# Kernel optimization log

Hardware: AMD Instinct MI355X
Metric: run time of the kernel (lower is better)

The kernel has to match this reference:

```python
import jax, jax.numpy as jnp
import numpy as np

S, G, N, E = 4, 3, 20000, 320000   # seq_len, num_graphs, nodes, edges
DIN = HID = OUT = 64


def setup_inputs() -> dict:
    key = jax.random.key(0)
    ks = jax.random.split(key, 12)
    s = 0.1  # weight scale ~ Glorot-ish for d=64
    return {
        "x": jax.random.normal(ks[0], (S, G, N, DIN), jnp.float32),
        "edge_index": jax.random.randint(ks[1], (S, G, 2, E), 0, N, dtype=jnp.int32),
        "W1l": jax.random.normal(ks[2], (G, DIN, HID), jnp.float32) * s,
        "W1r": jax.random.normal(ks[3], (G, DIN, HID), jnp.float32) * s,
        "b1": jnp.zeros((G, HID), jnp.float32),
        "W2l": jax.random.normal(ks[4], (G, HID, OUT), jnp.float32) * s,
        "W2r": jax.random.normal(ks[5], (G, HID, OUT), jnp.float32) * s,
        "b2": jnp.zeros((G, OUT), jnp.float32),
        "Wih": jax.random.normal(ks[6], (4 * OUT, OUT), jnp.float32) * s,
        "Whh": jax.random.normal(ks[7], (4 * OUT, OUT), jnp.float32) * s,
        "bih": jnp.zeros((4 * OUT,), jnp.float32),
        "bhh": jnp.zeros((4 * OUT,), jnp.float32),
    }


def _sage(x, ei, Wl, Wr, b):
    # PyG SAGEConv(aggr='mean'): out = mean_{j->i}(x_j) @ Wl + x_i @ Wr + b
    src, dst = ei[0], ei[1]
    n = x.shape[0]
    msg = jax.ops.segment_sum(x[src], dst, num_segments=n)          # [N, d]
    cnt = jax.ops.segment_sum(jnp.ones((ei.shape[1], 1), x.dtype), dst, num_segments=n)
    mean = jnp.where(cnt > 0, msg / jnp.maximum(cnt, 1.0), 0.0)
    return mean @ Wl + x @ Wr + b


def _gnn(x, ei, Wl1, Wr1, bb1, Wl2, Wr2, bb2):
    h = jnp.tanh(_sage(x, ei, Wl1, Wr1, bb1))
    return jnp.tanh(_sage(h, ei, Wl2, Wr2, bb2))


def reference(x, edge_index, W1l, W1r, b1, W2l, W2r, b2, Wih, Whh, bih, bhh):
    # vmap over graphs (each graph has its own conv weights), then over timesteps
    per_graph = jax.vmap(_gnn, in_axes=(0, 0, 0, 0, 0, 0, 0, 0))
    per_seq = jax.vmap(per_graph, in_axes=(0, 0, None, None, None, None, None, None))
    h = per_seq(x, edge_index, W1l, W1r, b1, W2l, W2r, b2)          # [S, G, N, OUT]
    # torch: per timestep stack graphs [G,N,O] -> transpose -> [N,G,O]; cat over seq on dim0
    lstm_in = jnp.transpose(h, (0, 2, 1, 3)).reshape(S * N, G, OUT)  # [B, T=G, OUT]
    B = lstm_in.shape[0]

    def step(carry, xt):
        hp, cp = carry
        gates = xt @ Wih.T + hp @ Whh.T + bih + bhh                 # [B, 4*OUT]
        i, f, g, o = jnp.split(gates, 4, axis=-1)                   # torch gate order i,f,g,o
        c = jax.nn.sigmoid(f) * cp + jax.nn.sigmoid(i) * jnp.tanh(g)
        hn = jax.nn.sigmoid(o) * jnp.tanh(c)
        return (hn, c), None

    init = (jnp.zeros((B, OUT), x.dtype), jnp.zeros((B, OUT), x.dtype))
    (h_last, _), _ = jax.lax.scan(step, init, jnp.transpose(lstm_in, (1, 0, 2)))
    return h_last  # [S*N, OUT] == lstm_out[:, -1, :].squeeze()
```

## Files before the change

### kernel.cpp

```cpp
#include <hip/hip_runtime.h>
#include <math.h>

#define S 4
#define G 3
#define NN 20000
#define EE 320000
#define D 64
#define SG (S*G)

#define RGS 32
#define RNODES2 625
#define BCAP 14336
#define CHUNKA 100

#define LTILES 313
#define LTASKS (12*LTILES)
#define LQ (LTASKS/8)
#define LR (LTASKS%8)
#define NGRP   (NN/16)

static __device__ __forceinline__ float rcpf(float x){ return __builtin_amdgcn_rcpf(x); }
static __device__ __forceinline__ float sigmf(float x){ return rcpf(1.0f + __expf(-x)); }
static __device__ __forceinline__ float tanhf_fast(float x){
    float t = __expf(2.0f*x);
    return 1.0f - 2.0f*rcpf(t + 1.0f);
}

static __device__ __forceinline__ unsigned short f2bf(float f){
    union { float f; unsigned u; } v; v.f = f;
    unsigned r = v.u + 0x7FFF + ((v.u >> 16) & 1);
    return (unsigned short)(r >> 16);
}

typedef short bf16x8 __attribute__((ext_vector_type(8)));
typedef float f32x4  __attribute__((ext_vector_type(4)));


__global__ __launch_bounds__(256) void binA_kernel(const int* __restrict__ ei,
                                                   int* __restrict__ bcur,
                                                   int* __restrict__ bkt){
    __shared__ int wcnt[4*RGS];
    __shared__ int wb[4*RGS];
    int chunk = blockIdx.x, sg = blockIdx.y;
    int tid = threadIdx.x, w = tid >> 6;
    const int* srcp = ei + (size_t)(sg*2 + 0)*EE;
    const int* dstp = ei + (size_t)(sg*2 + 1)*EE;
    const int EPC = EE/CHUNKA;
    int start = chunk*EPC, end = start + EPC;

    for (int it = 0; it < (EPC + 1023)/1024; ++it){
        if (tid < 4*RGS) wcnt[tid] = 0;
        __syncthreads();
        int e = start + it*1024 + tid*4;
        bool valid = e < end;
        int d_[4], s_[4], r_[4], dl_[4], rk_[4];
        if (valid){
            int4 d4 = *(const int4*)&dstp[e];
            int4 s4 = *(const int4*)&srcp[e];
            d_[0]=d4.x; d_[1]=d4.y; d_[2]=d4.z; d_[3]=d4.w;
            s_[0]=s4.x; s_[1]=s4.y; s_[2]=s4.z; s_[3]=s4.w;
            #pragma unroll
            for (int j = 0; j < 4; ++j){
                int r = d_[j] / RNODES2;
                r_[j]  = r;
                dl_[j] = d_[j] - r*RNODES2;
                rk_[j] = atomicAdd(&wcnt[w*RGS + r], 1);
            }
        }
        __syncthreads();
        if (tid < RGS){
            int c0 = wcnt[0*RGS+tid], c1 = wcnt[1*RGS+tid];
            int c2 = wcnt[2*RGS+tid], c3 = wcnt[3*RGS+tid];
            int tot = c0+c1+c2+c3;
            int gb = 0;
            if (tot > 0) gb = atomicAdd(&bcur[sg*RGS + tid], tot);
            wb[0*RGS+tid] = gb;
            wb[1*RGS+tid] = gb + c0;
            wb[2*RGS+tid] = gb + c0 + c1;
            wb[3*RGS+tid] = gb + c0 + c1 + c2;
        }
        __syncthreads();
        if (valid){
            #pragma unroll
            for (int j = 0; j < 4; ++j){
                int pos = wb[w*RGS + r_[j]] + rk_[j];
                if (pos < BCAP)
                    bkt[(size_t)(sg*RGS + r_[j])*BCAP + pos] = (dl_[j] << 15) | s_[j];
            }
        }
    }
}


__global__ __launch_bounds__(256) void buildB_kernel(int* __restrict__ bkt,
                                                     const int* __restrict__ bcur,
                                                     int* __restrict__ off2,
                                                     int* __restrict__ deg2,
                                                     int* __restrict__ nid2,
                                                     int* __restrict__ offU){
    __shared__ int hist[RNODES2];
    __shared__ int pref[RNODES2];
    __shared__ int seg[BCAP];
    __shared__ int sums[256];
    __shared__ int dh[64];
    int sg = blockIdx.x / RGS, rg = blockIdx.x % RGS;
    int tid = threadIdx.x;
    int cnt = bcur[sg*RGS + rg];
    if (cnt > BCAP) cnt = BCAP;
    size_t base = (size_t)(sg*RGS + rg)*BCAP;
    int gnode = sg*NN + rg*RNODES2;

    for (int i = tid; i < RNODES2; i += 256) hist[i] = 0;
    if (tid < 64) dh[tid] = 0;
    __syncthreads();
    for (int j = tid; j < cnt; j += 256)
        atomicAdd(&hist[bkt[base + j] >> 15], 1);
    __syncthreads();

    int lo = tid*3, hi = min(lo+3, RNODES2);
    int s = 0;
    for (int i = lo; i < hi; ++i) s += (hist[i] + 3) & ~3;
    sums[tid] = s; __syncthreads();
    for (int ofs = 1; ofs < 256; ofs <<= 1){
        int v = (tid >= ofs) ? sums[tid-ofs] : 0;
        __syncthreads();
        sums[tid] += v;
        __syncthreads();
    }
    int run = sums[tid] - s;
    for (int i = lo; i < hi; ++i){
        pref[i] = run;
        offU[gnode + i] = (int)base + run;
        run += (hist[i] + 3) & ~3;
    }
    __syncthreads();

    for (int i = tid; i < RNODES2; i += 256)
        atomicAdd(&dh[min(hist[i], 63)], 1);
    __syncthreads();
    if (tid == 0){
        int r = 0;
        for (int k = 0; k < 64; ++k){ int c = dh[k]; dh[k] = r; r += c; }
    }
    __syncthreads();
    for (int i = tid; i < RNODES2; i += 256){
        int pos = atomicAdd(&dh[min(hist[i], 63)], 1);
        off2[gnode + pos] = offU[gnode + i];
        deg2[gnode + pos] = hist[i];
        nid2[gnode + pos] = rg*RNODES2 + i;
    }
    __syncthreads();

    for (int j = tid; j < cnt; j += 256){
        int p = bkt[base + j];
        int slot = atomicAdd(&pref[p >> 15], 1);
        if (slot < BCAP) seg[slot] = p & 0x7FFF;
    }
    __syncthreads();

    int padtot = min(sums[255], BCAP);
    for (int j = tid; j < padtot; j += 256) bkt[base + j] = seg[j];
}


__global__ __launch_bounds__(256) void convert_kernel(const float* __restrict__ x,
                                                      unsigned short* __restrict__ xb){
    int idx = blockIdx.x*256 + threadIdx.x;
    if (idx >= SG*NN*16) return;
    float4 v = ((const float4*)x)[idx];
    uint2 pk;
    pk.x = (unsigned)f2bf(v.x) | ((unsigned)f2bf(v.y) << 16);
    pk.y = (unsigned)f2bf(v.z) | ((unsigned)f2bf(v.w) << 16);
    ((uint2*)xb)[idx] = pk;
}


__global__ __launch_bounds__(256) void wprep2_kernel(const float* __restrict__ W1l,
                                                     const float* __restrict__ W1r,
                                                     const float* __restrict__ W2l,
                                                     const float* __restrict__ W2r,
                                                     const float* __restrict__ Wih,
                                                     const float* __restrict__ Whh,
                                                     const float* __restrict__ bih,
                                                     const float* __restrict__ bhh,
                                                     unsigned short* __restrict__ WL1,
                                                     unsigned short* __restrict__ WL2,
                                                     unsigned short* __restrict__ Wt,
                                                     float* __restrict__ bc){
    int idx = blockIdx.x*256 + threadIdx.x;
    if (idx < 24576){
        int g = idx >> 13, rem = idx & 8191, col = rem >> 7, k = rem & 127;
        float v = (k < 64) ? W1l[((size_t)g*64 + k)*64 + col]
                           : W1r[((size_t)g*64 + (k-64))*64 + col];
        WL1[idx] = f2bf(v);
    } else if (idx < 49152){
        int t = idx - 24576;
        int g = t >> 13, rem = t & 8191, col = rem >> 7, k = rem & 127;
        float v = (k < 64) ? W2l[((size_t)g*64 + k)*64 + col]
                           : W2r[((size_t)g*64 + (k-64))*64 + col];
        WL2[t] = f2bf(v);
    } else if (idx < 81920){
        int t = idx - 49152;
        int col = t >> 7, k = t & 127;
        float v = (k < 64) ? Wih[col*64 + k] : Whh[col*64 + (k - 64)];
        Wt[t] = f2bf(v);
    } else if (idx < 82176){
        int t = idx - 81920;
        bc[t] = bih[t] + bhh[t];
    }
}


#define WP 72

#define LOADCH(F, IX, JB) { \
    int ii0_ = (IX).x, ii1_ = (IX).y, ii2_ = (IX).z, ii3_ = (IX).w; \
    unsigned o0_ = (((unsigned)ii0_) << 7) + qb; if ((JB) + 0 >= dg) o0_ = zoff; \
    unsigned o1_ = (((unsigned)ii1_) << 7) + qb; if ((JB) + 1 >= dg) o1_ = zoff; \
    unsigned o2_ = (((unsigned)ii2_) << 7) + qb; if ((JB) + 2 >= dg) o2_ = zoff; \
    unsigned o3_ = (((unsigned)ii3_) << 7) + qb; if ((JB) + 3 >= dg) o3_ = zoff; \
    F[0] = *(const bf16x8*)(inbc + o0_); F[1] = *(const bf16x8*)(inbc + o0_ + 64); \
    F[2] = *(const bf16x8*)(inbc + o1_); F[3] = *(const bf16x8*)(inbc + o1_ + 64); \
    F[4] = *(const bf16x8*)(inbc + o2_); F[5] = *(const bf16x8*)(inbc + o2_ + 64); \
    F[6] = *(const bf16x8*)(inbc + o3_); F[7] = *(const bf16x8*)(inbc + o3_ + 64); \
}

#define MFMAS(F) { \
    __builtin_amdgcn_s_setprio(1); \
    _Pragma("unroll") \
    for (int j_ = 0; j_ < 4; ++j_){ \
        _Pragma("unroll") \
        for (int ct_ = 0; ct_ < 4; ++ct_) \
            acc[ct_] = __builtin_amdgcn_mfma_f32_16x16x32_bf16(F[2*j_],   B0[ct_], acc[ct_], 0, 0, 0); \
        _Pragma("unroll") \
        for (int ct_ = 0; ct_ < 4; ++ct_) \
            acc[ct_] = __builtin_amdgcn_mfma_f32_16x16x32_bf16(F[2*j_+1], B1[ct_], acc[ct_], 0, 0, 0); \
    } \
    __builtin_amdgcn_s_setprio(0); \
}

__global__ __launch_bounds__(256,3) void layer_kernel(const unsigned short* __restrict__ xb,
                                                    const int* __restrict__ off2,
                                                    const int* __restrict__ deg2,
                                                    const int* __restrict__ nid2,
                                                    const int* __restrict__ csr,
                                                    const unsigned short* __restrict__ WL,
                                                    const float* __restrict__ bias,
                                                    unsigned short* __restrict__ outb){
    __shared__ unsigned short sO[4][16*WP];
    int L = blockIdx.x;
    int xcd = L & 7;
    int task = ((xcd < LR) ? xcd*(LQ+1) : LR*(LQ+1) + (xcd-LR)*LQ) + (L >> 3);
    int sg = task / LTILES;
    int tsel = task - sg*LTILES;
    int tile = (LTILES-1) - tsel;
    int g = sg % G;
    int tid = threadIdx.x;
    int wave = tid >> 6, lane = tid & 63;
    int r = lane & 15, q = lane >> 4;
    unsigned qb = (unsigned)(q << 4);
    const char* inbc = (const char*)(xb + (size_t)sg*NN*D);

    int gid = tile*4 + wave;
    bool wv = (gid < NGRP);

    const unsigned short* WLg = WL + (size_t)g*64*128;
    bf16x8 B0[4], B1[4];
    #pragma unroll
    for (int ct = 0; ct < 4; ++ct){
        B0[ct] = *(const bf16x8*)&WLg[(ct*16 + r)*128 + 0*32 + q*8];
        B1[ct] = *(const bf16x8*)&WLg[(ct*16 + r)*128 + 1*32 + q*8];
    }
    asm volatile("" : "+v"(B0[0]), "+v"(B0[1]), "+v"(B0[2]), "+v"(B0[3]),
                      "+v"(B1[0]), "+v"(B1[1]), "+v"(B1[2]), "+v"(B1[3]));

    int idx = sg*NN + gid*16 + r;
    int node = 0, dg = 0, a = 0;
    if (wv){
        node = nid2[idx];
        a    = off2[idx];
        dg   = deg2[idx];
    }
    int mx = dg;
    mx = max(mx, __shfl_xor(mx, 1));
    mx = max(mx, __shfl_xor(mx, 2));
    mx = max(mx, __shfl_xor(mx, 4));
    mx = max(mx, __shfl_xor(mx, 8));

    bf16x8 S0 = *(const bf16x8*)(inbc + (((unsigned)node) << 7) + qb);
    bf16x8 S1 = *(const bf16x8*)(inbc + (((unsigned)node) << 7) + qb + 64);

    unsigned zoff = (((unsigned)((SG - sg)*NN)) << 7) + qb;

    f32x4 acc[4];
    #pragma unroll
    for (int ct = 0; ct < 4; ++ct) acc[ct] = (f32x4){0.f,0.f,0.f,0.f};

    if (mx > 0){
        int4 ix0 = *(const int4*)&csr[a];
        int4 ix1 = *(const int4*)&csr[a + 4];
        bf16x8 FA[8], FB[8];
        LOADCH(FA, ix0, 0);
        LOADCH(FB, ix1, 4);
        ix0 = *(const int4*)&csr[a + 8];
        ix1 = *(const int4*)&csr[a + 12];
        int nch = (mx + 3) >> 2;
        for (int c = 0; c < nch; c += 2){
            MFMAS(FA);
            LOADCH(FA, ix0, (c + 2)*4);
            ix0 = *(const int4*)&csr[a + (c + 4)*4];
            if (c + 1 < nch){
                MFMAS(FB);
                LOADCH(FB, ix1, (c + 3)*4);
                ix1 = *(const int4*)&csr[a + (c + 5)*4];
            }
        }
    }

    float inv[4];
    #pragma unroll
    for (int reg = 0; reg < 4; ++reg){
        int d = __shfl(dg, (q << 2) | reg, 16);
        inv[reg] = (d > 0) ? rcpf((float)d) : 0.0f;
    }
    #pragma unroll
    for (int ct = 0; ct < 4; ++ct)
        #pragma unroll
        for (int reg = 0; reg < 4; ++reg)
            acc[ct][reg] *= inv[reg];

    #pragma unroll
    for (int ct = 0; ct < 4; ++ct){
        bf16x8 b2 = *(const bf16x8*)&WLg[(ct*16 + r)*128 + 2*32 + q*8];
        acc[ct] = __builtin_amdgcn_mfma_f32_16x16x32_bf16(S0, b2, acc[ct], 0, 0, 0);
        bf16x8 b3 = *(const bf16x8*)&WLg[(ct*16 + r)*128 + 3*32 + q*8];
        acc[ct] = __builtin_amdgcn_mfma_f32_16x16x32_bf16(S1, b3, acc[ct], 0, 0, 0);
    }

    #pragma unroll
    for (int ct = 0; ct < 4; ++ct){
        float bv = bias[g*64 + ct*16 + r];
        #pragma unroll
        for (int reg = 0; reg < 4; ++reg)
            sO[wave][(q*4+reg)*WP + ct*16 + r] = f2bf(tanhf_fast(acc[ct][reg] + bv));
    }
    if (wv){
        #pragma unroll
        for (int pass = 0; pass < 2; ++pass){
            int rloc = pass*8 + (lane >> 3), chunk = lane & 7;
            int i2 = gid*16 + rloc;
            int nd = nid2[sg*NN + i2];
            uint4 v = *(const uint4*)&sO[wave][rloc*WP + chunk*8];
            *(uint4*)&outb[((size_t)sg*NN + nd)*D + chunk*8] = v;
        }
    }
}


__global__ __launch_bounds__(256) void lstm_kernel(const unsigned short* __restrict__ h2b,
                                                   const unsigned short* __restrict__ Wt,
                                                   const float* __restrict__ bc,
                                                   float* __restrict__ out){
    __shared__ unsigned short sH[64*WP];
    int tid = threadIdx.x;
    int b0 = blockIdx.x * 64;
    int wave = tid >> 6, lane = tid & 63;
    int n0 = lane & 15, q = lane >> 4;
    int jcol = wave*16 + n0;

    float bb[4];
    #pragma unroll
    for (int T = 0; T < 4; ++T) bb[T] = bc[T*64 + jcol];

    float c[4][4];
    #pragma unroll
    for (int rt = 0; rt < 4; ++rt)
        #pragma unroll
        for (int reg = 0; reg < 4; ++reg) c[rt][reg] = 0.0f;

    int s_[4], n_[4];
    #pragma unroll
    for (int rt = 0; rt < 4; ++rt){
        int b = b0 + rt*16 + n0;
        s_[rt] = b / NN; n_[rt] = b - s_[rt]*NN;
    }

    #pragma unroll
    for (int t = 0; t < G; ++t){
        f32x4 accv[4][4];
        #pragma unroll
        for (int rt = 0; rt < 4; ++rt)
            #pragma unroll
            for (int T = 0; T < 4; ++T) accv[rt][T] = (f32x4){0.f,0.f,0.f,0.f};

        int nkc = (t == 0) ? 2 : 4;
        #pragma unroll
        for (int kc = 0; kc < 4; ++kc){
            if (kc >= nkc) break;
            bf16x8 af[4];
            #pragma unroll
            for (int rt = 0; rt < 4; ++rt){
                if (kc < 2) af[rt] = *(const bf16x8*)&h2b[((size_t)(s_[rt]*G + t)*NN + n_[rt])*D + kc*32 + q*8];
                else        af[rt] = *(const bf16x8*)&sH[(rt*16 + n0)*WP + (kc-2)*32 + q*8];
            }
            #pragma unroll
            for (int T = 0; T < 4; ++T){
                int ct = T*4 + wave;
                bf16x8 bfr = *(const bf16x8*)&Wt[(ct*16 + n0)*128 + kc*32 + q*8];
                #pragma unroll
                for (int rt = 0; rt < 4; ++rt)
                    accv[rt][T] = __builtin_amdgcn_mfma_f32_16x16x32_bf16(af[rt], bfr, accv[rt][T], 0, 0, 0);
            }
        }
        if (t > 0) __syncthreads();

        #pragma unroll
        for (int rt = 0; rt < 4; ++rt){
            #pragma unroll
            for (int reg = 0; reg < 4; ++reg){
                float ig = sigmf(accv[rt][0][reg] + bb[0]);
                float fg = sigmf(accv[rt][1][reg] + bb[1]);
                float gg = tanhf_fast(accv[rt][2][reg] + bb[2]);
                float og = sigmf(accv[rt][3][reg] + bb[3]);
                float cn = fg*c[rt][reg] + ig*gg;
                c[rt][reg] = cn;
                float hv = og * tanhf_fast(cn);
                int row = rt*16 + q*4 + reg;
                if (t < G-1) sH[row*WP + jcol] = f2bf(hv);
                else         out[(size_t)(b0 + row)*D + jcol] = hv;
            }
        }
        if (t < G-1) __syncthreads();
    }
}


extern "C" void kernel_launch(void* const* d_in, const int* in_sizes, int n_in,
                              void* d_out, int out_size, void* d_ws, size_t ws_size,
                              hipStream_t stream) {
    const float* x   = (const float*)d_in[0];
    const int*   ei  = (const int*)  d_in[1];
    const float* W1l = (const float*)d_in[2];
    const float* W1r = (const float*)d_in[3];
    const float* b1  = (const float*)d_in[4];
    const float* W2l = (const float*)d_in[5];
    const float* W2r = (const float*)d_in[6];
    const float* b2  = (const float*)d_in[7];
    const float* Wih = (const float*)d_in[8];
    const float* Whh = (const float*)d_in[9];
    const float* bih = (const float*)d_in[10];
    const float* bhh = (const float*)d_in[11];
    float* out = (float*)d_out;

    char* ws = (char*)d_ws;
    size_t cur = 0;
    auto alloc = [&](size_t bytes)->void*{
        cur = (cur + 255) & ~(size_t)255;
        void* p = ws + cur; cur += bytes; return p;
    };
    int*   bkt  = (int*)alloc((size_t)SG*RGS*BCAP*4);
    int*   bcur = (int*)alloc((size_t)SG*RGS*4);
    int*   off2 = (int*)alloc((size_t)SG*NN*4);
    int*   deg2 = (int*)alloc((size_t)SG*NN*4);
    int*   nid2 = (int*)alloc((size_t)SG*NN*4);
    int*   offU = (int*)alloc((size_t)SG*NN*4);
    unsigned short* xb  = (unsigned short*)alloc(((size_t)SG*NN + 1)*D*2);
    unsigned short* h1b = (unsigned short*)alloc(((size_t)SG*NN + 1)*D*2);
    unsigned short* h2b = (unsigned short*)alloc((size_t)SG*NN*D*2);
    unsigned short* WL1 = (unsigned short*)alloc((size_t)G*64*128*2);
    unsigned short* WL2 = (unsigned short*)alloc((size_t)G*64*128*2);
    unsigned short* Wt  = (unsigned short*)alloc((size_t)256*128*2);
    float* bc   = (float*)alloc((size_t)256*4);
    (void)ws_size; (void)in_sizes; (void)n_in; (void)out_size;

    (void)hipMemsetAsync(bcur, 0, (size_t)SG*RGS*4, stream);
    (void)hipMemsetAsync(xb  + (size_t)SG*NN*D, 0, (size_t)D*2, stream);
    (void)hipMemsetAsync(h1b + (size_t)SG*NN*D, 0, (size_t)D*2, stream);

    convert_kernel<<<(SG*NN*16 + 255)/256, 256, 0, stream>>>(x, xb);
    binA_kernel  <<<dim3(CHUNKA, SG), 256, 0, stream>>>(ei, bcur, bkt);
    buildB_kernel<<<SG*RGS, 256, 0, stream>>>(bkt, bcur, off2, deg2, nid2, offU);
    wprep2_kernel<<<321, 256, 0, stream>>>(W1l, W1r, W2l, W2r, Wih, Whh, bih, bhh,
                                           WL1, WL2, Wt, bc);

    layer_kernel<<<LTASKS, 256, 0, stream>>>(xb,  off2, deg2, nid2, bkt, WL1, b1, h1b);
    layer_kernel<<<LTASKS, 256, 0, stream>>>(h1b, off2, deg2, nid2, bkt, WL2, b2, h2b);

    lstm_kernel <<<(S*NN)/64, 256, 0, stream>>>(h2b, Wt, bc, out);
}
```

Before: 462.4 us.

## Aggregate neighbors via identity-matrix MFMA before weight GEMM instead of projecting each neighbor

```diff
diff --git a/kernel.cpp b/kernel.cpp
--- a/kernel.cpp
+++ b/kernel.cpp
@@ -213,33 +213,36 @@
 
 #define WP 72
 
-#define LOADCH(F, IX, JB) { \
-    int ii0_ = (IX).x, ii1_ = (IX).y, ii2_ = (IX).z, ii3_ = (IX).w; \
-    unsigned o0_ = (((unsigned)ii0_) << 7) + qb; if ((JB) + 0 >= dg) o0_ = zoff; \
-    unsigned o1_ = (((unsigned)ii1_) << 7) + qb; if ((JB) + 1 >= dg) o1_ = zoff; \
-    unsigned o2_ = (((unsigned)ii2_) << 7) + qb; if ((JB) + 2 >= dg) o2_ = zoff; \
-    unsigned o3_ = (((unsigned)ii3_) << 7) + qb; if ((JB) + 3 >= dg) o3_ = zoff; \
-    F[0] = *(const bf16x8*)(inbc + o0_); F[1] = *(const bf16x8*)(inbc + o0_ + 64); \
-    F[2] = *(const bf16x8*)(inbc + o1_); F[3] = *(const bf16x8*)(inbc + o1_ + 64); \
-    F[4] = *(const bf16x8*)(inbc + o2_); F[5] = *(const bf16x8*)(inbc + o2_ + 64); \
-    F[6] = *(const bf16x8*)(inbc + o3_); F[7] = *(const bf16x8*)(inbc + o3_ + 64); \
-}
-
-#define MFMAS(F) { \
-    __builtin_amdgcn_s_setprio(1); \
-    _Pragma("unroll") \
-    for (int j_ = 0; j_ < 4; ++j_){ \
-        _Pragma("unroll") \
-        for (int ct_ = 0; ct_ < 4; ++ct_) \
-            acc[ct_] = __builtin_amdgcn_mfma_f32_16x16x32_bf16(F[2*j_],   B0[ct_], acc[ct_], 0, 0, 0); \
-        _Pragma("unroll") \
-        for (int ct_ = 0; ct_ < 4; ++ct_) \
-            acc[ct_] = __builtin_amdgcn_mfma_f32_16x16x32_bf16(F[2*j_+1], B1[ct_], acc[ct_], 0, 0, 0); \
-    } \
-    __builtin_amdgcn_s_setprio(0); \
-}
-
-__global__ __launch_bounds__(256,3) void layer_kernel(const unsigned short* __restrict__ xb,
+#define LOADC(F, BASE) { \
+    int s0_ = (BASE) + (q >> 1); \
+    int s1_ = s0_ + 2; \
+    int n0_ = csr[a + s0_]; \
+    int n1_ = csr[a + s1_]; \
+    unsigned o0_ = (s0_ < dg) ? (((unsigned)n0_) << 7) : zoff0; \
+    unsigned o1_ = (s1_ < dg) ? (((unsigned)n1_) << 7) : zoff0; \
+    o0_ += qh; o1_ += qh; \
+    F[0] = *(const bf16x8*)(inbc + o0_); \
+    F[1] = *(const bf16x8*)(inbc + o0_ + 32); \
+    F[2] = *(const bf16x8*)(inbc + o0_ + 64); \
+    F[3] = *(const bf16x8*)(inbc + o0_ + 96); \
+    F[4] = *(const bf16x8*)(inbc + o1_); \
+    F[5] = *(const bf16x8*)(inbc + o1_ + 32); \
+    F[6] = *(const bf16x8*)(inbc + o1_ + 64); \
+    F[7] = *(const bf16x8*)(inbc + o1_ + 96); \
+}
+
+#define MFMA8(F) { \
+    acc[0] = __builtin_amdgcn_mfma_f32_16x16x32_bf16(F[0], BI, acc[0], 0, 0, 0); \
+    acc[1] = __builtin_amdgcn_mfma_f32_16x16x32_bf16(F[1], BI, acc[1], 0, 0, 0); \
+    acc[2] = __builtin_amdgcn_mfma_f32_16x16x32_bf16(F[2], BI, acc[2], 0, 0, 0); \
+    acc[3] = __builtin_amdgcn_mfma_f32_16x16x32_bf16(F[3], BI, acc[3], 0, 0, 0); \
+    acc[0] = __builtin_amdgcn_mfma_f32_16x16x32_bf16(F[4], BI, acc[0], 0, 0, 0); \
+    acc[1] = __builtin_amdgcn_mfma_f32_16x16x32_bf16(F[5], BI, acc[1], 0, 0, 0); \
+    acc[2] = __builtin_amdgcn_mfma_f32_16x16x32_bf16(F[6], BI, acc[2], 0, 0, 0); \
+    acc[3] = __builtin_amdgcn_mfma_f32_16x16x32_bf16(F[7], BI, acc[3], 0, 0, 0); \
+}
+
+__global__ __launch_bounds__(256,4) void layer_kernel(const unsigned short* __restrict__ xb,
                                                     const int* __restrict__ off2,
                                                     const int* __restrict__ deg2,
                                                     const int* __restrict__ nid2,
@@ -247,6 +250,7 @@
                                                     const unsigned short* __restrict__ WL,
                                                     const float* __restrict__ bias,
                                                     unsigned short* __restrict__ outb){
+    __shared__ unsigned short sM[4][16*WP];
     __shared__ unsigned short sO[4][16*WP];
     int L = blockIdx.x;
     int xcd = L & 7;
@@ -258,21 +262,23 @@
     int tid = threadIdx.x;
     int wave = tid >> 6, lane = tid & 63;
     int r = lane & 15, q = lane >> 4;
-    unsigned qb = (unsigned)(q << 4);
+    unsigned qh = (unsigned)((q & 1) << 4);
     const char* inbc = (const char*)(xb + (size_t)sg*NN*D);
 
     int gid = tile*4 + wave;
     bool wv = (gid < NGRP);
 
-    const unsigned short* WLg = WL + (size_t)g*64*128;
-    bf16x8 B0[4], B1[4];
-    #pragma unroll
-    for (int ct = 0; ct < 4; ++ct){
-        B0[ct] = *(const bf16x8*)&WLg[(ct*16 + r)*128 + 0*32 + q*8];
-        B1[ct] = *(const bf16x8*)&WLg[(ct*16 + r)*128 + 1*32 + q*8];
-    }
-    asm volatile("" : "+v"(B0[0]), "+v"(B0[1]), "+v"(B0[2]), "+v"(B0[3]),
-                      "+v"(B1[0]), "+v"(B1[1]), "+v"(B1[2]), "+v"(B1[3]));
+    union { uint4 u; bf16x8 v; } biu;
+    {
+        unsigned v_ = 0x3F80u << ((r & 1) * 16);
+        bool on = ((r >> 3) == (q & 1));
+        int w_ = (r & 7) >> 1;
+        biu.u.x = (on && w_ == 0) ? v_ : 0u;
+        biu.u.y = (on && w_ == 1) ? v_ : 0u;
+        biu.u.z = (on && w_ == 2) ? v_ : 0u;
+        biu.u.w = (on && w_ == 3) ? v_ : 0u;
+    }
+    bf16x8 BI = biu.v;
 
     int idx = sg*NN + gid*16 + r;
     int node = 0, dg = 0, a = 0;
@@ -287,32 +293,22 @@
     mx = max(mx, __shfl_xor(mx, 4));
     mx = max(mx, __shfl_xor(mx, 8));
 
-    bf16x8 S0 = *(const bf16x8*)(inbc + (((unsigned)node) << 7) + qb);
-    bf16x8 S1 = *(const bf16x8*)(inbc + (((unsigned)node) << 7) + qb + 64);
-
-    unsigned zoff = (((unsigned)((SG - sg)*NN)) << 7) + qb;
+    unsigned zoff0 = (((unsigned)((SG - sg)*NN)) << 7);
 
     f32x4 acc[4];
     #pragma unroll
-    for (int ct = 0; ct < 4; ++ct) acc[ct] = (f32x4){0.f,0.f,0.f,0.f};
+    for (int cb = 0; cb < 4; ++cb) acc[cb] = (f32x4){0.f,0.f,0.f,0.f};
 
     if (mx > 0){
-        int4 ix0 = *(const int4*)&csr[a];
-        int4 ix1 = *(const int4*)&csr[a + 4];
-        bf16x8 FA[8], FB[8];
-        LOADCH(FA, ix0, 0);
-        LOADCH(FB, ix1, 4);
-        ix0 = *(const int4*)&csr[a + 8];
-        ix1 = *(const int4*)&csr[a + 12];
         int nch = (mx + 3) >> 2;
+        bf16x8 Fa[8], Fb[8];
+        LOADC(Fa, 0);
         for (int c = 0; c < nch; c += 2){
-            MFMAS(FA);
-            LOADCH(FA, ix0, (c + 2)*4);
-            ix0 = *(const int4*)&csr[a + (c + 4)*4];
+            if (c + 1 < nch) LOADC(Fb, (c + 1)*4);
+            MFMA8(Fa);
             if (c + 1 < nch){
-                MFMAS(FB);
-                LOADCH(FB, ix1, (c + 3)*4);
-                ix1 = *(const int4*)&csr[a + (c + 5)*4];
+                if (c + 2 < nch) LOADC(Fa, (c + 2)*4);
+                MFMA8(Fb);
             }
         }
     }
@@ -324,17 +320,25 @@
         inv[reg] = (d > 0) ? rcpf((float)d) : 0.0f;
     }
     #pragma unroll
-    for (int ct = 0; ct < 4; ++ct)
+    for (int cb = 0; cb < 4; ++cb)
         #pragma unroll
         for (int reg = 0; reg < 4; ++reg)
-            acc[ct][reg] *= inv[reg];
-
-    #pragma unroll
-    for (int ct = 0; ct < 4; ++ct){
-        bf16x8 b2 = *(const bf16x8*)&WLg[(ct*16 + r)*128 + 2*32 + q*8];
-        acc[ct] = __builtin_amdgcn_mfma_f32_16x16x32_bf16(S0, b2, acc[ct], 0, 0, 0);
-        bf16x8 b3 = *(const bf16x8*)&WLg[(ct*16 + r)*128 + 3*32 + q*8];
-        acc[ct] = __builtin_amdgcn_mfma_f32_16x16x32_bf16(S1, b3, acc[ct], 0, 0, 0);
+            sM[wave][(q*4 + reg)*WP + cb*16 + r] = f2bf(acc[cb][reg] * inv[reg]);
+
+    const unsigned short* WLg = WL + (size_t)g*64*128;
+    f32x4 accv[4];
+    #pragma unroll
+    for (int ct = 0; ct < 4; ++ct) accv[ct] = (f32x4){0.f,0.f,0.f,0.f};
+    #pragma unroll
+    for (int kc = 0; kc < 4; ++kc){
+        bf16x8 af;
+        if (kc < 2) af = *(const bf16x8*)&sM[wave][r*WP + kc*32 + q*8];
+        else        af = *(const bf16x8*)(inbc + (((unsigned)node) << 7) + (unsigned)((kc-2)*64 + q*16));
+        #pragma unroll
+        for (int ct = 0; ct < 4; ++ct){
+            bf16x8 bfr = *(const bf16x8*)&WLg[(ct*16 + r)*128 + kc*32 + q*8];
+            accv[ct] = __builtin_amdgcn_mfma_f32_16x16x32_bf16(af, bfr, accv[ct], 0, 0, 0);
+        }
     }
 
     #pragma unroll
@@ -342,7 +346,7 @@
         float bv = bias[g*64 + ct*16 + r];
         #pragma unroll
         for (int reg = 0; reg < 4; ++reg)
-            sO[wave][(q*4+reg)*WP + ct*16 + r] = f2bf(tanhf_fast(acc[ct][reg] + bv));
+            sO[wave][(q*4+reg)*WP + ct*16 + r] = f2bf(tanhf_fast(accv[ct][reg] + bv));
     }
     if (wv){
         #pragma unroll
```

New measurement: 450.6 us. -2.6%, faster.
